# Optimization experiments

Measured on AMD Instinct MI355X. Metric: run time of the kernel, lower is better.

The kernel has to match this reference:

```python
import jax, jax.numpy as jnp
import numpy as np

N = 4096
D_IMG = 512
D_FEAT = 512
D_H = 256
D_Z = 128
N_CLS = 64
CHANGE_FRAC = 1.0  # alpha


def setup_inputs() -> dict:
    key = jax.random.key(0)
    ks = jax.random.split(key, 12)
    u = jax.random.uniform(ks[0], (N, N))
    a = (jnp.triu(u, 1) < 0.01).astype(jnp.float32)
    adj_ori = a + a.T
    i = jnp.arange(N)
    # GCN-normalized adjacency D^-1/2 (A+I) D^-1/2 (input to ep_net)
    a_hat = adj_ori.at[i, i].set(1.0)
    d = jnp.power(a_hat.sum(1), -0.5)
    adj_norm = a_hat * d[:, None] * d[None, :]
    xav = lambda k, s: jax.random.uniform(k, s, jnp.float32, -1.0, 1.0) * jnp.sqrt(6.0 / (s[0] + s[1]))
    return {
        "adj_norm": adj_norm,
        "adj_ori": adj_ori,
        "feats_ori": jax.random.normal(ks[1], (N, D_FEAT), jnp.float32),
        "img_feats": jax.random.normal(ks[2], (N, D_IMG), jnp.float32),
        "csd_ori": jax.random.normal(ks[3], (N_CLS, D_FEAT), jnp.float32),
        "csd_img": jax.random.normal(ks[4], (N_CLS, D_IMG), jnp.float32),
        "noise": jax.random.normal(ks[5], (N, D_Z), jnp.float32),
        "Wb": xav(ks[6], (D_IMG, D_H)),
        "Wm": xav(ks[7], (D_H, D_Z)),
        "Wl": xav(ks[8], (D_H, D_Z)),
        "fc1_W": xav(ks[9], (2 * D_FEAT, D_H)),
        "fc1_b": jnp.zeros((D_H,), jnp.float32),
        "fc2_W": xav(ks[10], (2 * D_H, D_IMG)),
        "fc2_b": jnp.zeros((D_IMG,), jnp.float32),
    }


def _ceil_st(x):
    # CeilNoGradient: ceil forward, identity backward (straight-through)
    return x + jax.lax.stop_gradient(jnp.ceil(x) - x)


def _gsage_layer(adj, h, W, b, relu):
    neigh = adj @ h
    mean_neigh = neigh / (adj.sum(axis=1, keepdims=True) + 1e-7)
    x = jnp.concatenate((h, mean_neigh), axis=1) @ W + b
    return jax.nn.relu(x) if relu else x


def _sample_adj_edge(adj_logits, adj):
    n_edges = jnp.sum(adj != 0)
    n_change = jnp.floor(n_edges.astype(jnp.float32) * CHANGE_FRAC / 2.0).astype(jnp.int32)
    ep = jnp.triu(adj_logits, 1)
    ep = ep - jnp.min(ep)
    ep = ep / jnp.max(ep)
    T = N * N
    # --- remove lowest-prob existing edges ---
    mask_rm = ep * adj
    v = jnp.sort(mask_rm.reshape(-1))  # ascending; positives at the tail
    n_nz = jnp.sum(v > 0)
    n_rm = jnp.minimum(n_nz, n_change)
    thresh_rm = v[T - n_nz + n_rm - 1]  # n_rm-th smallest positive
    mask_rm = jnp.where(mask_rm > thresh_rm, 0.0, mask_rm)
    mask_rm = _ceil_st(mask_rm)
    mask_rm = mask_rm + mask_rm.T
    adj_new = adj - mask_rm
    # --- add highest-prob missing edges ---
    mask_add = ep * (1.0 - adj)
    v2 = jnp.sort(mask_add.reshape(-1))
    n_nz2 = jnp.sum(v2 > 0)
    n_add = jnp.minimum(n_nz2, n_change)
    thresh_add = v2[T - n_add]  # n_add-th largest positive
    mask_add = jnp.where(mask_add < thresh_add, 0.0, mask_add)
    mask_add = _ceil_st(mask_add)
    mask_add = mask_add + mask_add.T
    return adj_new + mask_add


def reference(adj_norm, adj_ori, feats_ori, img_feats, csd_ori, csd_img, noise,
              Wb, Wm, Wl, fc1_W, fc1_b, fc2_W, fc2_b):
    # ep_net (VGAE, gae=False)
    hidden = adj_norm @ (img_feats @ Wb)
    mean = jax.nn.relu(adj_norm @ (hidden @ Wm))
    logstd = jax.nn.relu(adj_norm @ (hidden @ Wl))
    Z = noise * jnp.exp(logstd) + mean
    adj_logits = Z @ Z.T
    # edge rewiring
    adj_new = _sample_adj_edge(adj_logits, adj_ori)
    # normalize_adj for 'gsage': fill diag 1, L1 row-normalize
    i = jnp.arange(N)
    adj_new = adj_new.at[i, i].set(1.0)
    adj_new = adj_new / jnp.maximum(jnp.sum(jnp.abs(adj_new), axis=1, keepdims=True), 1e-12)
    # nc_net (DGPN)
    preds_img = img_feats @ csd_img.T
    h1 = _gsage_layer(adj_new, feats_ori, fc1_W, fc1_b, relu=True)
    h2 = _gsage_layer(adj_new, h1, fc2_W, fc2_b, relu=False)
    feat_total = jax.nn.log_softmax(h2, axis=-1)
    preds_total = feat_total @ csd_img.T
    return preds_total, feat_total, preds_img, adj_logits
```

## Files before the change

kernel.cpp:

```cpp
#include <hip/hip_runtime.h>
#include <type_traits>
#include <stdint.h>

#define NN 4096
#define TTOT 16777216UL

enum { F_RELU=1, F_ACC=2, F_RS=4, F_BIAS=8 };

struct SelParams {
  unsigned min_ord, max_ord, n_up;
  float lo, M, c0;
  unsigned n_change, rm_prefix, rm_k, add_prefix, add_k;
  float t_rm, t_add;
  unsigned hist_rm[256], hist_add[256];
};

__device__ __forceinline__ unsigned ordenc(float x){
  unsigned u = __float_as_uint(x);
  return (u & 0x80000000u) ? ~u : (u | 0x80000000u);
}
__device__ __forceinline__ float orddec(unsigned o){
  unsigned u = (o & 0x80000000u) ? (o ^ 0x80000000u) : ~u;
  return __uint_as_float(u);
}
__device__ __forceinline__ float orddec_ok(unsigned o){
  unsigned u = (o & 0x80000000u) ? (o ^ 0x80000000u) : ~o;
  return __uint_as_float(u);
}

__global__ __launch_bounds__(256)
void k_gemm8s(const signed char* __restrict__ A, const float* __restrict__ B,
              float* __restrict__ C0, float* __restrict__ C1,
              float* __restrict__ C2, float* __restrict__ C3, int N)
{
  __shared__ float As[32][68];
  __shared__ float Bs[32][68];
  const int t  = threadIdx.x;
  const int tx = t & 15, ty = t >> 4;
  const int m0 = blockIdx.y * 64, n0 = blockIdx.x * 64;
  const int kz = blockIdx.z;
  const int kbase = kz * 1024;
  float* C = (kz == 0) ? C0 : (kz == 1) ? C1 : (kz == 2) ? C2 : C3;
  const int mA = t >> 2, kA = (t & 3) * 8;
  const int kB = t >> 4, nB = (t & 15) * 4;
  float acc[4][4] = {};
  int2   a_r  = *reinterpret_cast<const int2*>(A + (size_t)(m0+mA)*4096 + kbase + kA);
  float4 b_r0 = *reinterpret_cast<const float4*>(B + (size_t)(kbase+kB)*N + n0 + nB);
  float4 b_r1 = *reinterpret_cast<const float4*>(B + (size_t)(kbase+kB+16)*N + n0 + nB);
  for (int k0 = 0; k0 < 1024; k0 += 32) {
    {
      int u0 = a_r.x, u1 = a_r.y;
      #pragma unroll
      for (int b = 0; b < 4; ++b){
        As[kA+b  ][mA] = (float)(int)(signed char)((u0 >> (8*b)) & 0xff);
        As[kA+4+b][mA] = (float)(int)(signed char)((u1 >> (8*b)) & 0xff);
      }
      Bs[kB   ][nB+0]=b_r0.x; Bs[kB   ][nB+1]=b_r0.y; Bs[kB   ][nB+2]=b_r0.z; Bs[kB   ][nB+3]=b_r0.w;
      Bs[kB+16][nB+0]=b_r1.x; Bs[kB+16][nB+1]=b_r1.y; Bs[kB+16][nB+2]=b_r1.z; Bs[kB+16][nB+3]=b_r1.w;
    }
    __syncthreads();
    if (k0 + 32 < 1024){
      a_r  = *reinterpret_cast<const int2*>(A + (size_t)(m0+mA)*4096 + kbase + (k0+32) + kA);
      b_r0 = *reinterpret_cast<const float4*>(B + (size_t)(kbase+k0+32+kB)*N + n0 + nB);
      b_r1 = *reinterpret_cast<const float4*>(B + (size_t)(kbase+k0+48+kB)*N + n0 + nB);
    }
    #pragma unroll
    for (int kk = 0; kk < 32; ++kk) {
      float4 av = *reinterpret_cast<const float4*>(&As[kk][ty*4]);
      float4 bv = *reinterpret_cast<const float4*>(&Bs[kk][tx*4]);
      float a[4]={av.x,av.y,av.z,av.w};
      float b[4]={bv.x,bv.y,bv.z,bv.w};
      #pragma unroll
      for (int i=0;i<4;++i)
        #pragma unroll
        for (int j=0;j<4;++j)
          acc[i][j] = fmaf(a[i], b[j], acc[i][j]);
    }
    __syncthreads();
  }
  #pragma unroll
  for (int i=0;i<4;++i){
    float* cp = C + (size_t)(m0 + ty*4 + i)*N + (n0 + tx*4);
    *reinterpret_cast<float4*>(cp) = make_float4(acc[i][0],acc[i][1],acc[i][2],acc[i][3]);
  }
}

__global__ __launch_bounds__(256)
void k_add4(const float* __restrict__ A, const float* __restrict__ B,
            const float* __restrict__ C, const float* __restrict__ D,
            float* __restrict__ O, int n4)
{
  int i = blockIdx.x*256 + threadIdx.x;
  if (i < n4){
    float4 a = reinterpret_cast<const float4*>(A)[i];
    float4 b = reinterpret_cast<const float4*>(B)[i];
    float4 c = reinterpret_cast<const float4*>(C)[i];
    float4 d = reinterpret_cast<const float4*>(D)[i];
    reinterpret_cast<float4*>(O)[i] = make_float4(((a.x+b.x)+c.x)+d.x,
                                                  ((a.y+b.y)+c.y)+d.y,
                                                  ((a.z+b.z)+c.z)+d.z,
                                                  ((a.w+b.w)+c.w)+d.w);
  }
}

template<typename TA>
__global__ __launch_bounds__(256)
void k_gemm32(const TA* __restrict__ A, const float* __restrict__ B,
              float* __restrict__ C, int M, int N, int K, int ldc,
              const float* __restrict__ rowscale, const float* __restrict__ bias,
              int flags)
{
  __shared__ float As[16][36];
  __shared__ float Bs[16][68];
  const int t  = threadIdx.x;
  const int tx = t & 15, ty = t >> 4;
  const int m0 = blockIdx.y * 32, n0 = blockIdx.x * 64;
  float acc[2][4] = {};
  for (int k0 = 0; k0 < K; k0 += 16) {
    if (t < 128){
      const int mA = t >> 2, kA = (t & 3) * 4;
      if constexpr (std::is_same<TA, float>::value) {
        float4 v = *reinterpret_cast<const float4*>(A + (size_t)(m0+mA)*K + (k0+kA));
        As[kA+0][mA]=v.x; As[kA+1][mA]=v.y; As[kA+2][mA]=v.z; As[kA+3][mA]=v.w;
      } else {
        int u = *reinterpret_cast<const int*>(A + (size_t)(m0+mA)*K + (k0+kA));
        As[kA+0][mA]=(float)(int)(signed char)( u       & 0xff);
        As[kA+1][mA]=(float)(int)(signed char)((u>>8)   & 0xff);
        As[kA+2][mA]=(float)(int)(signed char)((u>>16)  & 0xff);
        As[kA+3][mA]=(float)(int)(signed char)((u>>24)  & 0xff);
      }
    }
    {
      const int kB = t >> 4, nB = (t & 15) * 4;
      float4 w = *reinterpret_cast<const float4*>(B + (size_t)(k0+kB)*N + (n0+nB));
      Bs[kB][nB+0]=w.x; Bs[kB][nB+1]=w.y; Bs[kB][nB+2]=w.z; Bs[kB][nB+3]=w.w;
    }
    __syncthreads();
    #pragma unroll
    for (int kk = 0; kk < 16; ++kk) {
      float a0 = As[kk][ty*2+0];
      float a1 = As[kk][ty*2+1];
      float4 bv = *reinterpret_cast<const float4*>(&Bs[kk][tx*4]);
      float b[4]={bv.x,bv.y,bv.z,bv.w};
      #pragma unroll
      for (int j=0;j<4;++j){
        acc[0][j] = fmaf(a0, b[j], acc[0][j]);
        acc[1][j] = fmaf(a1, b[j], acc[1][j]);
      }
    }
    __syncthreads();
  }
  #pragma unroll
  for (int i=0;i<2;++i){
    const int m = m0 + ty*2 + i;
    const float rsv = (flags & F_RS) ? rowscale[m] : 1.0f;
    float* cp = C + (size_t)m*ldc + (n0 + tx*4);
    float o[4];
    #pragma unroll
    for (int j=0;j<4;++j){
      float v = acc[i][j] * rsv;
      if (flags & F_BIAS) v += bias[n0 + tx*4 + j];
      if (flags & F_ACC)  v += cp[j];
      if (flags & F_RELU) v = fmaxf(v, 0.0f);
      o[j] = v;
    }
    *reinterpret_cast<float4*>(cp) = make_float4(o[0],o[1],o[2],o[3]);
  }
}

__global__ __launch_bounds__(256)
void k_gemm32T(const float* __restrict__ A, const float* __restrict__ B,
               float* __restrict__ C, int M, int N, int K, int ldc)
{
  __shared__ float As[16][36];
  __shared__ float Bs[16][68];
  const int t  = threadIdx.x;
  const int tx = t & 15, ty = t >> 4;
  const int m0 = blockIdx.y * 32, n0 = blockIdx.x * 64;
  float acc[2][4] = {};
  for (int k0 = 0; k0 < K; k0 += 16) {
    if (t < 128){
      const int mA = t >> 2, kA = (t & 3) * 4;
      float4 v = *reinterpret_cast<const float4*>(A + (size_t)(m0+mA)*K + (k0+kA));
      As[kA+0][mA]=v.x; As[kA+1][mA]=v.y; As[kA+2][mA]=v.z; As[kA+3][mA]=v.w;
    }
    {
      const int nB = t >> 2, kB = (t & 3) * 4;
      float4 w = *reinterpret_cast<const float4*>(B + (size_t)(n0+nB)*K + (k0+kB));
      Bs[kB+0][nB]=w.x; Bs[kB+1][nB]=w.y; Bs[kB+2][nB]=w.z; Bs[kB+3][nB]=w.w;
    }
    __syncthreads();
    #pragma unroll
    for (int kk = 0; kk < 16; ++kk) {
      float a0 = As[kk][ty*2+0];
      float a1 = As[kk][ty*2+1];
      float4 bv = *reinterpret_cast<const float4*>(&Bs[kk][tx*4]);
      float b[4]={bv.x,bv.y,bv.z,bv.w};
      #pragma unroll
      for (int j=0;j<4;++j){
        acc[0][j] = fmaf(a0, b[j], acc[0][j]);
        acc[1][j] = fmaf(a1, b[j], acc[1][j]);
      }
    }
    __syncthreads();
  }
  #pragma unroll
  for (int i=0;i<2;++i){
    const int m = m0 + ty*2 + i;
    float* cp = C + (size_t)m*ldc + (n0 + tx*4);
    *reinterpret_cast<float4*>(cp) = make_float4(acc[i][0],acc[i][1],acc[i][2],acc[i][3]);
  }
}

__global__ __launch_bounds__(256)
void k_fc(const float* __restrict__ A1, const float* __restrict__ B1,
          const float* __restrict__ bias,
          const float* __restrict__ A2, const float* __restrict__ B2,
          const float* __restrict__ rowscale,
          float* __restrict__ C, int N, int K1, int K2, int relu)
{
  __shared__ float As[16][36];
  __shared__ float Bs[16][68];
  const int t  = threadIdx.x;
  const int tx = t & 15, ty = t >> 4;
  const int m0 = blockIdx.y * 32, n0 = blockIdx.x * 64;
  float acc1[2][4] = {};
  float acc2[2][4] = {};
  for (int k0 = 0; k0 < K1; k0 += 16) {
    if (t < 128){
      const int mA = t >> 2, kA = (t & 3) * 4;
      float4 v = *reinterpret_cast<const float4*>(A1 + (size_t)(m0+mA)*K1 + (k0+kA));
      As[kA+0][mA]=v.x; As[kA+1][mA]=v.y; As[kA+2][mA]=v.z; As[kA+3][mA]=v.w;
    }
    {
      const int kB = t >> 4, nB = (t & 15) * 4;
      float4 w = *reinterpret_cast<const float4*>(B1 + (size_t)(k0+kB)*N + (n0+nB));
      Bs[kB][nB+0]=w.x; Bs[kB][nB+1]=w.y; Bs[kB][nB+2]=w.z; Bs[kB][nB+3]=w.w;
    }
    __syncthreads();
    #pragma unroll
    for (int kk = 0; kk < 16; ++kk) {
      float a0 = As[kk][ty*2+0];
      float a1 = As[kk][ty*2+1];
      float4 bv = *reinterpret_cast<const float4*>(&Bs[kk][tx*4]);
      float b[4]={bv.x,bv.y,bv.z,bv.w};
      #pragma unroll
      for (int j=0;j<4;++j){
        acc1[0][j] = fmaf(a0, b[j], acc1[0][j]);
        acc1[1][j] = fmaf(a1, b[j], acc1[1][j]);
      }
    }
    __syncthreads();
  }
  for (int k0 = 0; k0 < K2; k0 += 16) {
    if (t < 128){
      const int mA = t >> 2, kA = (t & 3) * 4;
      float4 v = *reinterpret_cast<const float4*>(A2 + (size_t)(m0+mA)*K2 + (k0+kA));
      As[kA+0][mA]=v.x; As[kA+1][mA]=v.y; As[kA+2][mA]=v.z; As[kA+3][mA]=v.w;
    }
    {
      const int kB = t >> 4, nB = (t & 15) * 4;
      float4 w = *reinterpret_cast<const float4*>(B2 + (size_t)(k0+kB)*N + (n0+nB));
      Bs[kB][nB+0]=w.x; Bs[kB][nB+1]=w.y; Bs[kB][nB+2]=w.z; Bs[kB][nB+3]=w.w;
    }
    __syncthreads();
    #pragma unroll
    for (int kk = 0; kk < 16; ++kk) {
      float a0 = As[kk][ty*2+0];
      float a1 = As[kk][ty*2+1];
      float4 bv = *reinterpret_cast<const float4*>(&Bs[kk][tx*4]);
      float b[4]={bv.x,bv.y,bv.z,bv.w};
      #pragma unroll
      for (int j=0;j<4;++j){
        acc2[0][j] = fmaf(a0, b[j], acc2[0][j]);
        acc2[1][j] = fmaf(a1, b[j], acc2[1][j]);
      }
    }
    __syncthreads();
  }
  #pragma unroll
  for (int i=0;i<2;++i){
    const int m = m0 + ty*2 + i;
    const float rsv = rowscale[m];
    float* cp = C + (size_t)m*N + (n0 + tx*4);
    float o[4];
    #pragma unroll
    for (int j=0;j<4;++j){
      float t1 = acc1[i][j] + bias[n0 + tx*4 + j];
      float v  = acc2[i][j] * rsv;
      v += t1;
      if (relu) v = fmaxf(v, 0.0f);
      o[j] = v;
    }
    *reinterpret_cast<float4*>(cp) = make_float4(o[0],o[1],o[2],o[3]);
  }
}

__global__ __launch_bounds__(256)
void k_wcat(const float* __restrict__ Wm, const float* __restrict__ Wl,
            float* __restrict__ Wcat)
{
  int idx = blockIdx.x*256 + threadIdx.x;
  int row = idx >> 8, col = idx & 255;
  Wcat[idx] = (col < 128) ? Wm[row*128 + col] : Wl[row*128 + (col - 128)];
}

template<int D>
__global__ __launch_bounds__(256)
void k_spmmF(const float* __restrict__ A, const float* __restrict__ B,
             float* __restrict__ C)
{
  const int row = blockIdx.x, t = threadIdx.x;
  const int lane = t & 63, wv = t >> 6;
  __shared__ int   sc[288];
  __shared__ float sv[288];
  __shared__ int wtot[4];
  __shared__ int nsh;
  const float4* r4 = reinterpret_cast<const float4*>(A + (size_t)row*NN) + t*4;
  float lv[16];
  #pragma unroll
  for (int q=0;q<4;++q){
    float4 v = r4[q];
    lv[q*4+0]=v.x; lv[q*4+1]=v.y; lv[q*4+2]=v.z; lv[q*4+3]=v.w;
  }
  int c = 0;
  #pragma unroll
  for (int k=0;k<16;++k) c += (lv[k] != 0.0f);
  int inc = c;
  #pragma unroll
  for (int off=1; off<64; off<<=1){
    int v = __shfl_up(inc, off, 64);
    if (lane >= off) inc += v;
  }
  if (lane == 63) wtot[wv] = inc;
  __syncthreads();
  int wbase = 0;
  #pragma unroll
  for (int ww=0; ww<3; ++ww) if (ww < wv) wbase += wtot[ww];
  int pos = wbase + inc - c;
  #pragma unroll
  for (int k=0;k<16;++k){
    if (lv[k] != 0.0f){
      if (pos >= 0 && pos < 288){ sc[pos] = t*16+k; sv[pos] = lv[k]; }
      pos++;
    }
  }
  if (t == 255){
    int tot = wbase + inc;
    nsh = (tot < 288) ? tot : 288;
  }
  __syncthreads();
  const int n = nsh;
  float acc = 0.f;
  int s = 0;
  for (; s+4 <= n; s += 4){
    float x0 = B[(size_t)sc[s+0]*D + t];
    float x1 = B[(size_t)sc[s+1]*D + t];
    float x2 = B[(size_t)sc[s+2]*D + t];
    float x3 = B[(size_t)sc[s+3]*D + t];
    acc = fmaf(sv[s+0], x0, acc);
    acc = fmaf(sv[s+1], x1, acc);
    acc = fmaf(sv[s+2], x2, acc);
    acc = fmaf(sv[s+3], x3, acc);
  }
  for (; s < n; ++s) acc = fmaf(sv[s], B[(size_t)sc[s]*D + t], acc);
  C[(size_t)row*D + t] = acc;
}

__global__ __launch_bounds__(256)
void k_zzt(const float* __restrict__ Z, float* __restrict__ C)
{
  const int bx = blockIdx.x, by = blockIdx.y;
  if (by > bx) return;
  __shared__ float As[16][68];
  __shared__ float Bs[16][68];
  const int t = threadIdx.x, tx = t & 15, ty = t >> 4;
  const int m0 = by*64, n0 = bx*64;
  const int mA = t >> 2, kA = (t & 3) * 4;
  float acc[4][4] = {};
  for (int k0 = 0; k0 < 128; k0 += 16){
    float4 va = *reinterpret_cast<const float4*>(Z + (size_t)(m0+mA)*128 + k0 + kA);
    As[kA+0][mA]=va.x; As[kA+1][mA]=va.y; As[kA+2][mA]=va.z; As[kA+3][mA]=va.w;
    float4 vb = *reinterpret_cast<const float4*>(Z + (size_t)(n0+mA)*128 + k0 + kA);
    Bs[kA+0][mA]=vb.x; Bs[kA+1][mA]=vb.y; Bs[kA+2][mA]=vb.z; Bs[kA+3][mA]=vb.w;
    __syncthreads();
    #pragma unroll
    for (int kk = 0; kk < 16; ++kk) {
      float4 av = *reinterpret_cast<const float4*>(&As[kk][ty*4]);
      float4 bv = *reinterpret_cast<const float4*>(&Bs[kk][tx*4]);
      float a[4]={av.x,av.y,av.z,av.w};
      float b[4]={bv.x,bv.y,bv.z,bv.w};
      #pragma unroll
      for (int i=0;i<4;++i)
        #pragma unroll
        for (int j=0;j<4;++j)
          acc[i][j] = fmaf(a[i], b[j], acc[i][j]);
    }
    __syncthreads();
  }
  #pragma unroll
  for (int i=0;i<4;++i){
    float* cp = C + (size_t)(m0+ty*4+i)*NN + (n0 + tx*4);
    *reinterpret_cast<float4*>(cp) = make_float4(acc[i][0],acc[i][1],acc[i][2],acc[i][3]);
  }
  if (bx != by){
    for (int c0 = 0; c0 < 64; c0 += 16){
      __syncthreads();
      if (tx >= c0/4 && tx < c0/4 + 4){
        #pragma unroll
        for (int i=0;i<4;++i)
          #pragma unroll
          for (int j=0;j<4;++j)
            As[tx*4 + j - c0][ty*4 + i] = acc[i][j];
      }
      __syncthreads();
      const int c = t & 63, r0 = t >> 6;
      #pragma unroll
      for (int rr = 0; rr < 4; ++rr)
        C[(size_t)(n0 + c0 + r0 + rr*4)*NN + m0 + c] = As[r0 + rr*4][c];
    }
  }
}

__global__ __launch_bounds__(256)
void k_z2(const float* __restrict__ MPLP, const float* __restrict__ noise,
          float* __restrict__ Z)
{
  int i = blockIdx.x*256 + threadIdx.x;
  int m = i >> 7, c = i & 127;
  float mp = fmaxf(MPLP[(size_t)m*256 + c], 0.0f);
  float lp = fmaxf(MPLP[(size_t)m*256 + 128 + c], 0.0f);
  Z[i] = noise[i]*expf(lp) + mp;
}

__global__ __launch_bounds__(256)
void k_initstats(SelParams* p)
{
  int t = threadIdx.x;
  if (t == 0){
    p->min_ord = 0xFFFFFFFFu; p->max_ord = 0u; p->n_up = 0u;
    p->rm_prefix = 0u; p->add_prefix = 0u;
  }
  p->hist_rm[t] = 0u; p->hist_add[t] = 0u;
}

__global__ __launch_bounds__(256)
void k_stats1(const float* __restrict__ L, const float* __restrict__ adj,
              unsigned long long* __restrict__ mask, SelParams* __restrict__ p)
{
  unsigned mn=0xFFFFFFFFu, mx=0u, cnt=0u;
  size_t g = (size_t)blockIdx.x*256 + threadIdx.x;
  const size_t stride = (size_t)gridDim.x*256;
  for (; g < 262144; g += stride){
    const int i  = (int)(g >> 6);
    const int jb = (int)(g & 63) << 6;
    unsigned long long m = 0ull;
    if (jb + 63 > i){
      const float4* a4 = reinterpret_cast<const float4*>(adj + (size_t)i*NN + jb);
      const float4* l4 = reinterpret_cast<const float4*>(L   + (size_t)i*NN + jb);
      for (int w = 0; w < 16; ++w){
        const int j0 = jb + w*4;
        if (j0 + 3 <= i) continue;
        float4 av = a4[w]; float4 lv = l4[w];
        float ae[4]={av.x,av.y,av.z,av.w};
        float le[4]={lv.x,lv.y,lv.z,lv.w};
        #pragma unroll
        for (int e=0;e<4;++e){
          const int jj = j0 + e;
          if (jj > i){
            if (ae[e] != 0.0f){ m |= 1ull << (jj & 63); cnt++; }
            unsigned o = ordenc(le[e]);
            mn = (o < mn) ? o : mn;
            mx = (o > mx) ? o : mx;
          }
        }
      }
    }
    mask[g] = m;
  }
  __shared__ unsigned smn[256], smx[256], sc[256];
  int t = threadIdx.x;
  smn[t]=mn; smx[t]=mx; sc[t]=cnt; __syncthreads();
  for (int s=128; s>0; s>>=1){
    if (t < s){
      smn[t] = (smn[t+s] < smn[t]) ? smn[t+s] : smn[t];
      smx[t] = (smx[t+s] > smx[t]) ? smx[t+s] : smx[t];
      sc[t] += sc[t+s];
    }
    __syncthreads();
  }
  if (t == 0){
    atomicMin(&p->min_ord, smn[0]);
    atomicMax(&p->max_ord, smx[0]);
    atomicAdd(&p->n_up, sc[0]);
  }
}

__global__ void k_stats2(SelParams* p)
{
  float mnv = orddec_ok(p->min_ord), mxv = orddec_ok(p->max_ord);
  float lo = fminf(mnv, 0.0f), hi = fmaxf(mxv, 0.0f);
  p->lo = lo;
  p->M  = hi - lo;
  p->c0 = (0.0f - lo) / p->M;
  p->n_change = p->n_up;
}

__global__ __launch_bounds__(256)
void k_hist2(const float* __restrict__ L, const unsigned long long* __restrict__ mask,
             SelParams* __restrict__ p, int shift)
{
  __shared__ unsigned hr[256], ha[256];
  const int t = threadIdx.x;
  hr[t]=0u; ha[t]=0u; __syncthreads();
  const float lo = p->lo, Mv = p->M;
  const unsigned pr = p->rm_prefix, pa = p->add_prefix;
  const float4* L4 = reinterpret_cast<const float4*>(L);
  size_t q = (size_t)blockIdx.x*256 + t;
  const size_t stride = (size_t)gridDim.x*256;
  for (; q < TTOT/4; q += stride){
    const int i = (int)(q >> 10);
    const int j = (int)(q & 1023) << 2;
    if (j + 3 <= i) continue;
    float4 l = L4[q];
    const unsigned long long w = mask[q >> 4];
    float le[4]={l.x,l.y,l.z,l.w};
    #pragma unroll
    for (int e=0;e<4;++e){
      const int jj = j + e;
      if (jj <= i) continue;
      const unsigned key = __float_as_uint((le[e] - lo) / Mv);
      if (key == 0u) continue;
      const bool edge = (w >> (jj & 63)) & 1ull;
      if (edge){
        if (shift == 24 || (key >> (shift+8)) == pr) atomicAdd(&hr[(key>>shift)&255u], 1u);
      } else {
        if (shift == 24 || (key >> (shift+8)) == pa) atomicAdd(&ha[(key>>shift)&255u], 1u);
      }
    }
  }
  __syncthreads();
  if (hr[t]) atomicAdd(&p->hist_rm[t], hr[t]);
  if (ha[t]) atomicAdd(&p->hist_add[t], ha[t]);
}

__global__ __launch_bounds__(256)
void k_scan2(SelParams* __restrict__ p, int shift)
{
  const int t = threadIdx.x;
  if (t == 0){
    const unsigned c0k  = __float_as_uint(p->c0);
    const unsigned n_up = p->n_up;
    {
      unsigned injb = 300u, inj = 0u;
      if (c0k != 0u && (shift == 24 || (c0k >> (shift+8)) == p->rm_prefix)){
        injb = (c0k >> shift) & 255u; inj = n_up;
      }
      unsigned k;
      if (shift == 24){
        unsigned tot = inj;
        for (int d=0; d<256; ++d) tot += p->hist_rm[d];
        k = (tot < p->n_change) ? tot : p->n_change;
      } else k = p->rm_k;
      unsigned cum = 0u, digit = 255u;
      for (int d=0; d<256; ++d){
        unsigned hd = p->hist_rm[d] + (((unsigned)d == injb) ? inj : 0u);
        if (cum + hd >= k){ digit = (unsigned)d; k -= cum; break; }
        cum += hd;
      }
      p->rm_prefix = (p->rm_prefix << 8) | digit;
      p->rm_k = k;
      if (shift == 0) p->t_rm = __uint_as_float(p->rm_prefix);
    }
    {
      unsigned injb = 300u, inj = 0u;
      if (c0k != 0u && (shift == 24 || (c0k >> (shift+8)) == p->add_prefix)){
        injb = (c0k >> shift) & 255u;
        inj  = 8386560u - n_up + 4096u;
      }
      unsigned k;
      if (shift == 24){
        unsigned tot = inj;
        for (int d=0; d<256; ++d) tot += p->hist_add[d];
        k = (tot < p->n_change) ? tot : p->n_change;
      } else k = p->add_k;
      unsigned cum = 0u, digit = 0u;
      for (int d=255; d>=0; --d){
        unsigned hd = p->hist_add[d] + (((unsigned)d == injb) ? inj : 0u);
        if (cum + hd >= k){ digit = (unsigned)d; k -= cum; break; }
        cum += hd;
      }
      p->add_prefix = (p->add_prefix << 8) | digit;
      p->add_k = k;
      if (shift == 0) p->t_add = __uint_as_float(p->add_prefix);
    }
  }
  __syncthreads();
  p->hist_rm[t] = 0u; p->hist_add[t] = 0u;
}

__device__ __forceinline__ int adjval(bool edge, float v, float c0v, float trm, float tad)
{
  int rmU = (edge && v   >  0.0f && v   <= trm) ? 1 : 0;
  int rmL = (edge && c0v >  0.0f && c0v <= trm) ? 1 : 0;
  int adU = (!edge && v   >= tad) ? 1 : 0;
  int adL = (!edge && c0v >= tad) ? 1 : 0;
  return (edge ? 1 : 0) - rmU - rmL + adU + adL;
}

__global__ __launch_bounds__(256)
void k_apply(const float* __restrict__ L, const unsigned long long* __restrict__ mask,
             const SelParams* __restrict__ p, signed char* __restrict__ A8)
{
  const int bx = blockIdx.x, by = blockIdx.y;
  if (by > bx) return;
  const float lo=p->lo, Mv=p->M, c0v=p->c0, trm=p->t_rm, tad=p->t_add;
  const int i0 = by*64, j0 = bx*64, t = threadIdx.x;
  __shared__ signed char Vs[64][65];
  if (bx == by){
    for (int it=0; it<16; ++it){
      int e = it*256 + t; int r = e>>6, c = e&63;
      size_t idx = (size_t)(i0+r)*NN + (j0+c);
      if (r < c){
        bool edge = (mask[idx>>6] >> ((j0+c) & 63)) & 1ull;
        float v = (L[idx] - lo) / Mv;
        int val = adjval(edge, v, c0v, trm, tad);
        A8[idx] = (signed char)val;
        Vs[c][r] = (signed char)val;
      } else if (r == c){
        A8[idx] = 1;
      }
    }
    __syncthreads();
    for (int it=0; it<16; ++it){
      int e = it*256 + t; int r = e>>6, c = e&63;
      if (r > c) A8[(size_t)(i0+r)*NN + (j0+c)] = Vs[r][c];
    }
  } else {
    for (int it=0; it<16; ++it){
      int e = it*256 + t; int r = e>>6, c = e&63;
      size_t idx = (size_t)(i0+r)*NN + (j0+c);
      bool edge = (mask[idx>>6] >> ((j0+c) & 63)) & 1ull;
      float v = (L[idx] - lo) / Mv;
      int val = adjval(edge, v, c0v, trm, tad);
      A8[idx] = (signed char)val;
      Vs[c][r] = (signed char)val;
    }
    __syncthreads();
    for (int it=0; it<16; ++it){
      int e = it*256 + t; int r = e>>6, c = e&63;
      A8[(size_t)(j0+r)*NN + (i0+c)] = Vs[r][c];
    }
  }
}

__global__ __launch_bounds__(256)
void k_rowsum8(const signed char* __restrict__ A8, float* __restrict__ s_mean)
{
  const int row = blockIdx.x, t = threadIdx.x;
  const int4 w = reinterpret_cast<const int4*>(A8 + (size_t)row*NN)[t];
  int s = 0, a = 0;
  int vs[4] = {w.x, w.y, w.z, w.w};
  #pragma unroll
  for (int q=0; q<4; ++q){
    int u = vs[q];
    #pragma unroll
    for (int b=0; b<4; ++b){
      int c = (int)(signed char)((u >> (8*b)) & 0xff);
      s += c; a += (c < 0) ? -c : c;
    }
  }
  __shared__ int rs_[256], ra_[256];
  rs_[t]=s; ra_[t]=a; __syncthreads();
  for (int st=128; st>0; st>>=1){
    if (t < st){ rs_[t]+=rs_[t+st]; ra_[t]+=ra_[t+st]; }
    __syncthreads();
  }
  if (t == 0){
    float rs = (float)rs_[0], ra = (float)ra_[0];
    float A = fmaxf(ra, 1e-12f);
    s_mean[row] = (1.0f / A) / (rs / A + 1e-7f);
  }
}

__global__ __launch_bounds__(256)
void k_lsm(float* __restrict__ X)
{
  const int row = blockIdx.x, t = threadIdx.x;
  float* x = X + (size_t)row*512;
  float v0 = x[t], v1 = x[t+256];
  __shared__ float red[256];
  red[t] = fmaxf(v0, v1); __syncthreads();
  for (int s=128; s>0; s>>=1){
    if (t < s) red[t] = fmaxf(red[t], red[t+s]);
    __syncthreads();
  }
  float m = red[0]; __syncthreads();
  red[t] = expf(v0-m) + expf(v1-m); __syncthreads();
  for (int s=128; s>0; s>>=1){
    if (t < s) red[t] += red[t+s];
    __syncthreads();
  }
  float ls = logf(red[0]);
  x[t]     = (v0 - m) - ls;
  x[t+256] = (v1 - m) - ls;
}

extern "C" void kernel_launch(void* const* d_in, const int* in_sizes, int n_in,
                              void* d_out, int out_size, void* d_ws, size_t ws_size,
                              hipStream_t stream)
{
  (void)in_sizes; (void)n_in; (void)out_size; (void)ws_size;
  const float* adj_norm = (const float*)d_in[0];
  const float* adj_ori  = (const float*)d_in[1];
  const float* feats    = (const float*)d_in[2];
  const float* img      = (const float*)d_in[3];
  const float* csd_img  = (const float*)d_in[5];
  const float* noise    = (const float*)d_in[6];
  const float* Wb       = (const float*)d_in[7];
  const float* Wm       = (const float*)d_in[8];
  const float* Wl       = (const float*)d_in[9];
  const float* fc1W     = (const float*)d_in[10];
  const float* fc1b     = (const float*)d_in[11];
  const float* fc2W     = (const float*)d_in[12];
  const float* fc2b     = (const float*)d_in[13];

  float* out    = (float*)d_out;
  float* out_pt = out;
  float* out_ft = out + 262144;
  float* out_pi = out + 2359296;
  float* out_lg = out + 2621440;

  char* W = (char*)d_ws;
  signed char* adj8 = (signed char*)W;
  float* bufA   = (float*)(W + (16u<<20));
  float* bufB   = (float*)(W + (24u<<20));
  float* HMHL   = (float*)(W + (28u<<20));
  float* MPLP   = (float*)(W + (32u<<20));
  float* reg28  = HMHL;
  float* Z      = (float*)(W + (36u<<20));
  unsigned long long* mask = (unsigned long long*)(W + (38u<<20));
  float* reg36  = Z;
  float* s_mean = (float*)(W + (44u<<20));
  SelParams* sp = (SelParams*)(W + (44u<<20) + 65536);
  float* Wcat   = (float*)(W + (45u<<20));

  dim3 B(256);
  auto G32 = [](int M, int N){ return dim3((unsigned)(N/64), (unsigned)(M/32)); };

  k_gemm32<float><<<G32(4096,256),B,0,stream>>>(img, Wb, bufA, 4096,256,512,256, nullptr,nullptr,0);
  k_spmmF<256><<<4096,B,0,stream>>>(adj_norm, bufA, bufB);
  k_wcat<<<256,B,0,stream>>>(Wm, Wl, Wcat);
  k_gemm32<float><<<G32(4096,256),B,0,stream>>>(bufB, Wcat, HMHL, 4096,256,256,256, nullptr,nullptr,0);
  k_spmmF<256><<<4096,B,0,stream>>>(adj_norm, HMHL, MPLP);
  k_z2<<<2048,B,0,stream>>>(MPLP, noise, Z);
  k_zzt<<<dim3(64,64),B,0,stream>>>(Z, out_lg);

  k_initstats<<<1,B,0,stream>>>(sp);
  k_stats1<<<1024,B,0,stream>>>(out_lg, adj_ori, mask, sp);
  k_stats2<<<1,1,0,stream>>>(sp);
  for (int shift = 24; shift >= 0; shift -= 8){
    k_hist2<<<2048,B,0,stream>>>(out_lg, mask, sp, shift);
    k_scan2<<<1,B,0,stream>>>(sp, shift);
  }
  k_apply<<<dim3(64,64),B,0,stream>>>(out_lg, mask, sp, adj8);

  k_rowsum8<<<4096,B,0,stream>>>(adj8, s_mean);

  k_gemm8s<<<dim3(512/64, 64, 4),B,0,stream>>>(adj8, feats, bufA, reg28, out_ft, reg36, 512);
  k_add4<<<2048,B,0,stream>>>(bufA, reg28, out_ft, reg36, bufA, 524288);
  k_fc<<<G32(4096,256),B,0,stream>>>(feats, fc1W, fc1b, bufA, fc1W + 512*256, s_mean,
                                     bufB, 256, 512, 512, 1);
  k_gemm8s<<<dim3(256/64, 64, 4),B,0,stream>>>(adj8, bufB, reg28, MPLP, reg36, reg36 + 1048576, 256);
  k_add4<<<1024,B,0,stream>>>(reg28, MPLP, reg36, reg36 + 1048576, bufA, 262144);
  k_fc<<<G32(4096,512),B,0,stream>>>(bufB, fc2W, fc2b, bufA, fc2W + 256*512, s_mean,
                                     out_ft, 512, 256, 256, 0);
  k_lsm<<<4096,B,0,stream>>>(out_ft);

  k_gemm32T<<<G32(4096,64),B,0,stream>>>(out_ft, csd_img, out_pt, 4096,64,512,64);
  k_gemm32T<<<G32(4096,64),B,0,stream>>>(img, csd_img, out_pi, 4096,64,512,64);
}
```

Baseline: 1.018 ms.

## Use bf16 MFMA with three-way split operands for adjacency aggregation GEMMs

Replaces the FP32 split-K SIMT GEMM over the int8 rewired adjacency, and its four-way partial-sum add kernel, with a bf16 MFMA GEMM. The dense right-hand operand is first transposed and split into high, mid and low bf16 parts, so three MFMAs together keep close to FP32 accuracy while the int8 adjacency values convert exactly to bf16. This targets the FMA-bound aggregation step and removes the separate reduction pass. In exchange it adds a transpose/split pass, triples the B-operand traffic, and drops split-K, leaving fewer blocks (256 and 512) with a full 4096-long K loop each.

```diff
diff --git a/kernel.cpp b/kernel.cpp
--- a/kernel.cpp
+++ b/kernel.cpp
@@ -6,6 +6,10 @@
 #define TTOT 16777216UL
 
 enum { F_RELU=1, F_ACC=2, F_RS=4, F_BIAS=8 };
+
+typedef unsigned short ushort_t;
+using bf16x8 = __attribute__((ext_vector_type(8))) short;
+using f32x4  = __attribute__((ext_vector_type(4))) float;
 
 struct SelParams {
   unsigned min_ord, max_ord, n_up;
@@ -19,87 +23,122 @@
   unsigned u = __float_as_uint(x);
   return (u & 0x80000000u) ? ~u : (u | 0x80000000u);
 }
-__device__ __forceinline__ float orddec(unsigned o){
-  unsigned u = (o & 0x80000000u) ? (o ^ 0x80000000u) : ~u;
-  return __uint_as_float(u);
-}
 __device__ __forceinline__ float orddec_ok(unsigned o){
   unsigned u = (o & 0x80000000u) ? (o ^ 0x80000000u) : ~o;
   return __uint_as_float(u);
 }
-
-__global__ __launch_bounds__(256)
-void k_gemm8s(const signed char* __restrict__ A, const float* __restrict__ B,
-              float* __restrict__ C0, float* __restrict__ C1,
-              float* __restrict__ C2, float* __restrict__ C3, int N)
-{
-  __shared__ float As[32][68];
-  __shared__ float Bs[32][68];
-  const int t  = threadIdx.x;
-  const int tx = t & 15, ty = t >> 4;
+__device__ __forceinline__ ushort_t f2bf(float x){
+  unsigned u = __float_as_uint(x);
+  return (ushort_t)((u + 0x7FFFu + ((u >> 16) & 1u)) >> 16);
+}
+__device__ __forceinline__ float bf2f(ushort_t h){
+  return __uint_as_float(((unsigned)h) << 16);
+}
+
+template<int DN>
+__global__ __launch_bounds__(256)
+void k_b3t(const float* __restrict__ Bsrc, ushort_t* __restrict__ H,
+           ushort_t* __restrict__ Mg, ushort_t* __restrict__ L)
+{
+  __shared__ ushort_t sh[64][65], sm[64][65], sl[64][65];
+  const int t = threadIdx.x;
+  const int n0 = blockIdx.x * 64, k0 = blockIdx.y * 64;
+  #pragma unroll
+  for (int it = 0; it < 16; ++it){
+    int idx = it*256 + t; int r = idx >> 6, c = idx & 63;
+    float x  = Bsrc[(size_t)(k0 + r)*DN + n0 + c];
+    ushort_t hb = f2bf(x);
+    float r1 = x - bf2f(hb);
+    ushort_t mb = f2bf(r1);
+    float r2 = r1 - bf2f(mb);
+    ushort_t lb = f2bf(r2);
+    sh[r][c] = hb; sm[r][c] = mb; sl[r][c] = lb;
+  }
+  __syncthreads();
+  #pragma unroll
+  for (int it = 0; it < 16; ++it){
+    int idx = it*256 + t; int r = idx >> 6, c = idx & 63;
+    size_t o = (size_t)(n0 + r)*4096 + k0 + c;
+    H[o] = sh[c][r]; Mg[o] = sm[c][r]; L[o] = sl[c][r];
+  }
+}
+
+__global__ __launch_bounds__(256)
+void k_mfma(const signed char* __restrict__ A8,
+            const ushort_t* __restrict__ BH, const ushort_t* __restrict__ BM2,
+            const ushort_t* __restrict__ BL, float* __restrict__ C, int N)
+{
+  __shared__ ushort_t Ab[64][72];
+  __shared__ ushort_t Bb[3][64][72];
+  const int t = threadIdx.x;
   const int m0 = blockIdx.y * 64, n0 = blockIdx.x * 64;
-  const int kz = blockIdx.z;
-  const int kbase = kz * 1024;
-  float* C = (kz == 0) ? C0 : (kz == 1) ? C1 : (kz == 2) ? C2 : C3;
-  const int mA = t >> 2, kA = (t & 3) * 8;
-  const int kB = t >> 4, nB = (t & 15) * 4;
-  float acc[4][4] = {};
-  int2   a_r  = *reinterpret_cast<const int2*>(A + (size_t)(m0+mA)*4096 + kbase + kA);
-  float4 b_r0 = *reinterpret_cast<const float4*>(B + (size_t)(kbase+kB)*N + n0 + nB);
-  float4 b_r1 = *reinterpret_cast<const float4*>(B + (size_t)(kbase+kB+16)*N + n0 + nB);
-  for (int k0 = 0; k0 < 1024; k0 += 32) {
+  const int sr = t >> 2, sc = (t & 3) * 16;
+  const int w = t >> 6, lane = t & 63;
+  const int fr = lane & 15, fg = lane >> 4;
+
+  int4 a_r = *reinterpret_cast<const int4*>(A8 + (size_t)(m0+sr)*4096 + sc);
+  const ushort_t* bsrc0 = BH  + (size_t)(n0+sr)*4096 + sc;
+  const ushort_t* bsrc1 = BM2 + (size_t)(n0+sr)*4096 + sc;
+  const ushort_t* bsrc2 = BL  + (size_t)(n0+sr)*4096 + sc;
+  int4 b0a = reinterpret_cast<const int4*>(bsrc0)[0], b0b = reinterpret_cast<const int4*>(bsrc0)[1];
+  int4 b1a = reinterpret_cast<const int4*>(bsrc1)[0], b1b = reinterpret_cast<const int4*>(bsrc1)[1];
+  int4 b2a = reinterpret_cast<const int4*>(bsrc2)[0], b2b = reinterpret_cast<const int4*>(bsrc2)[1];
+
+  f32x4 acc[4][3];
+  #pragma unroll
+  for (int c = 0; c < 4; ++c)
+    #pragma unroll
+    for (int p = 0; p < 3; ++p)
+      acc[c][p] = (f32x4){0.f, 0.f, 0.f, 0.f};
+
+  for (int k0 = 0; k0 < 4096; k0 += 64){
     {
-      int u0 = a_r.x, u1 = a_r.y;
+      alignas(16) ushort_t tmp[16];
+      const signed char* ab = reinterpret_cast<const signed char*>(&a_r);
       #pragma unroll
-      for (int b = 0; b < 4; ++b){
-        As[kA+b  ][mA] = (float)(int)(signed char)((u0 >> (8*b)) & 0xff);
-        As[kA+4+b][mA] = (float)(int)(signed char)((u1 >> (8*b)) & 0xff);
-      }
-      Bs[kB   ][nB+0]=b_r0.x; Bs[kB   ][nB+1]=b_r0.y; Bs[kB   ][nB+2]=b_r0.z; Bs[kB   ][nB+3]=b_r0.w;
-      Bs[kB+16][nB+0]=b_r1.x; Bs[kB+16][nB+1]=b_r1.y; Bs[kB+16][nB+2]=b_r1.z; Bs[kB+16][nB+3]=b_r1.w;
-    }
-    __syncthreads();
-    if (k0 + 32 < 1024){
-      a_r  = *reinterpret_cast<const int2*>(A + (size_t)(m0+mA)*4096 + kbase + (k0+32) + kA);
-      b_r0 = *reinterpret_cast<const float4*>(B + (size_t)(kbase+k0+32+kB)*N + n0 + nB);
-      b_r1 = *reinterpret_cast<const float4*>(B + (size_t)(kbase+k0+48+kB)*N + n0 + nB);
-    }
-    #pragma unroll
-    for (int kk = 0; kk < 32; ++kk) {
-      float4 av = *reinterpret_cast<const float4*>(&As[kk][ty*4]);
-      float4 bv = *reinterpret_cast<const float4*>(&Bs[kk][tx*4]);
-      float a[4]={av.x,av.y,av.z,av.w};
-      float b[4]={bv.x,bv.y,bv.z,bv.w};
+      for (int i = 0; i < 16; ++i) tmp[i] = f2bf((float)(int)ab[i]);
+      *reinterpret_cast<int4*>(&Ab[sr][sc])     = reinterpret_cast<int4*>(tmp)[0];
+      *reinterpret_cast<int4*>(&Ab[sr][sc + 8]) = reinterpret_cast<int4*>(tmp)[1];
+      *reinterpret_cast<int4*>(&Bb[0][sr][sc])     = b0a;
+      *reinterpret_cast<int4*>(&Bb[0][sr][sc + 8]) = b0b;
+      *reinterpret_cast<int4*>(&Bb[1][sr][sc])     = b1a;
+      *reinterpret_cast<int4*>(&Bb[1][sr][sc + 8]) = b1b;
+      *reinterpret_cast<int4*>(&Bb[2][sr][sc])     = b2a;
+      *reinterpret_cast<int4*>(&Bb[2][sr][sc + 8]) = b2b;
+    }
+    __syncthreads();
+    if (k0 + 64 < 4096){
+      a_r = *reinterpret_cast<const int4*>(A8 + (size_t)(m0+sr)*4096 + (k0+64) + sc);
+      const ushort_t* p0 = BH  + (size_t)(n0+sr)*4096 + (k0+64) + sc;
+      const ushort_t* p1 = BM2 + (size_t)(n0+sr)*4096 + (k0+64) + sc;
+      const ushort_t* p2 = BL  + (size_t)(n0+sr)*4096 + (k0+64) + sc;
+      b0a = reinterpret_cast<const int4*>(p0)[0]; b0b = reinterpret_cast<const int4*>(p0)[1];
+      b1a = reinterpret_cast<const int4*>(p1)[0]; b1b = reinterpret_cast<const int4*>(p1)[1];
+      b2a = reinterpret_cast<const int4*>(p2)[0]; b2b = reinterpret_cast<const int4*>(p2)[1];
+    }
+    #pragma unroll
+    for (int kk = 0; kk < 64; kk += 32){
+      bf16x8 af = *reinterpret_cast<const bf16x8*>(&Ab[w*16 + fr][kk + fg*8]);
       #pragma unroll
-      for (int i=0;i<4;++i)
-        #pragma unroll
-        for (int j=0;j<4;++j)
-          acc[i][j] = fmaf(a[i], b[j], acc[i][j]);
-    }
-    __syncthreads();
-  }
-  #pragma unroll
-  for (int i=0;i<4;++i){
-    float* cp = C + (size_t)(m0 + ty*4 + i)*N + (n0 + tx*4);
-    *reinterpret_cast<float4*>(cp) = make_float4(acc[i][0],acc[i][1],acc[i][2],acc[i][3]);
-  }
-}
-
-__global__ __launch_bounds__(256)
-void k_add4(const float* __restrict__ A, const float* __restrict__ B,
-            const float* __restrict__ C, const float* __restrict__ D,
-            float* __restrict__ O, int n4)
-{
-  int i = blockIdx.x*256 + threadIdx.x;
-  if (i < n4){
-    float4 a = reinterpret_cast<const float4*>(A)[i];
-    float4 b = reinterpret_cast<const float4*>(B)[i];
-    float4 c = reinterpret_cast<const float4*>(C)[i];
-    float4 d = reinterpret_cast<const float4*>(D)[i];
-    reinterpret_cast<float4*>(O)[i] = make_float4(((a.x+b.x)+c.x)+d.x,
-                                                  ((a.y+b.y)+c.y)+d.y,
-                                                  ((a.z+b.z)+c.z)+d.z,
-                                                  ((a.w+b.w)+c.w)+d.w);
+      for (int c = 0; c < 4; ++c){
+        const int bn = c*16 + fr;
+        bf16x8 bh = *reinterpret_cast<const bf16x8*>(&Bb[0][bn][kk + fg*8]);
+        acc[c][0] = __builtin_amdgcn_mfma_f32_16x16x32_bf16(af, bh, acc[c][0], 0, 0, 0);
+        bf16x8 bm = *reinterpret_cast<const bf16x8*>(&Bb[1][bn][kk + fg*8]);
+        acc[c][1] = __builtin_amdgcn_mfma_f32_16x16x32_bf16(af, bm, acc[c][1], 0, 0, 0);
+        bf16x8 bl = *reinterpret_cast<const bf16x8*>(&Bb[2][bn][kk + fg*8]);
+        acc[c][2] = __builtin_amdgcn_mfma_f32_16x16x32_bf16(af, bl, acc[c][2], 0, 0, 0);
+      }
+    }
+    __syncthreads();
+  }
+  #pragma unroll
+  for (int c = 0; c < 4; ++c){
+    f32x4 s = acc[c][0] + acc[c][1];
+    s = s + acc[c][2];
+    #pragma unroll
+    for (int r = 0; r < 4; ++r)
+      C[(size_t)(m0 + w*16 + fg*4 + r)*N + n0 + c*16 + fr] = s[r];
   }
 }
 
@@ -737,13 +776,17 @@
   float* bufB   = (float*)(W + (24u<<20));
   float* HMHL   = (float*)(W + (28u<<20));
   float* MPLP   = (float*)(W + (32u<<20));
-  float* reg28  = HMHL;
   float* Z      = (float*)(W + (36u<<20));
   unsigned long long* mask = (unsigned long long*)(W + (38u<<20));
-  float* reg36  = Z;
   float* s_mean = (float*)(W + (44u<<20));
   SelParams* sp = (SelParams*)(W + (44u<<20) + 65536);
   float* Wcat   = (float*)(W + (45u<<20));
+  ushort_t* BT1h = (ushort_t*)(W + (28u<<20));
+  ushort_t* BT1m = (ushort_t*)(W + (32u<<20));
+  ushort_t* BT1l = (ushort_t*)(W + (36u<<20));
+  ushort_t* BT2h = (ushort_t*)(W + (28u<<20));
+  ushort_t* BT2m = (ushort_t*)(W + (30u<<20));
+  ushort_t* BT2l = (ushort_t*)(W + (32u<<20));
 
   dim3 B(256);
   auto G32 = [](int M, int N){ return dim3((unsigned)(N/64), (unsigned)(M/32)); };
@@ -767,12 +810,12 @@
 
   k_rowsum8<<<4096,B,0,stream>>>(adj8, s_mean);
 
-  k_gemm8s<<<dim3(512/64, 64, 4),B,0,stream>>>(adj8, feats, bufA, reg28, out_ft, reg36, 512);
-  k_add4<<<2048,B,0,stream>>>(bufA, reg28, out_ft, reg36, bufA, 524288);
+  k_b3t<512><<<dim3(8,64),B,0,stream>>>(feats, BT1h, BT1m, BT1l);
+  k_mfma<<<dim3(8,64),B,0,stream>>>(adj8, BT1h, BT1m, BT1l, bufA, 512);
   k_fc<<<G32(4096,256),B,0,stream>>>(feats, fc1W, fc1b, bufA, fc1W + 512*256, s_mean,
                                      bufB, 256, 512, 512, 1);
-  k_gemm8s<<<dim3(256/64, 64, 4),B,0,stream>>>(adj8, bufB, reg28, MPLP, reg36, reg36 + 1048576, 256);
-  k_add4<<<1024,B,0,stream>>>(reg28, MPLP, reg36, reg36 + 1048576, bufA, 262144);
+  k_b3t<256><<<dim3(4,64),B,0,stream>>>(bufB, BT2h, BT2m, BT2l);
+  k_mfma<<<dim3(4,64),B,0,stream>>>(adj8, BT2h, BT2m, BT2l, bufA, 256);
   k_fc<<<G32(4096,512),B,0,stream>>>(bufB, fc2W, fc2b, bufA, fc2W + 256*512, s_mean,
                                      out_ft, 512, 256, 256, 0);
   k_lsm<<<4096,B,0,stream>>>(out_ft);
```

After: 855.4 us. 1.19x faster.
